# Kernel optimization log

Hardware: AMD Instinct MI355X
Metric: run time of the kernel (lower is better)

## Reference

```python
import jax, jax.numpy as jnp
import numpy as np

B, S, BERT_H = 8, 512, 432
NL, HD = 12, 64
H = NL * HD  # 768
NEG = -1e12

def _lin(k, i, o):
    return jax.random.normal(k, (i, o), jnp.float32) * 0.02

def setup_inputs():
    key = jax.random.key(0)
    ks = jax.random.split(key, 12)
    return {
        "bert_hidden": jax.random.normal(ks[0], (B, S, BERT_H), jnp.float32),
        "attention_mask": jnp.ones((B, S), jnp.float32),
        "dense_w": _lin(ks[1], BERT_H, H), "dense_b": jnp.zeros((H,)),
        "sat_qw": _lin(ks[2], H, H), "sat_qb": jnp.zeros((H,)),
        "sat_kw": _lin(ks[3], H, H), "sat_kb": jnp.zeros((H,)),
        "sat_vw": _lin(ks[4], H, H), "sat_vb": jnp.zeros((H,)),
        "sat_ow": _lin(ks[5], H, H), "sat_ob": jnp.zeros((H,)),
        "rel_qw": _lin(ks[6], H, H), "rel_qb": jnp.zeros((H,)),
        "rel_kw": _lin(ks[7], H, H), "rel_kb": jnp.zeros((H,)),
        "rel_vw": _lin(ks[8], H, H), "rel_vb": jnp.zeros((H,)),
        "rel_ow": _lin(ks[9], H, H), "rel_ob": jnp.zeros((H,)),
        "lns_w": jnp.ones((H,)), "lns_b": jnp.zeros((H,)),
        "lnr_w": jnp.ones((H,)), "lnr_b": jnp.zeros((H,)),
        "head_w": _lin(ks[10], H, 2 * HD), "head_b": jnp.zeros((2 * HD,)),
        "tail_w": _lin(ks[11], 2 * HD, 2 * NL), "tail_b": jnp.zeros((2 * NL,)),
    }

def _layernorm(x, w, b, eps=1e-12):
    u = x.mean(-1, keepdims=True)
    s = ((x - u) ** 2).mean(-1, keepdims=True)
    return w * (x - u) / jnp.sqrt(s + eps) + b

def _mha(q_in, k_in, v_in, wq, bq, wk, bk, wv, bv, wo, bo):
    # q_in: [N, Lq, H]; k_in/v_in: [N, Lk, H]; dropout is identity (eval)
    N, Lq, _ = q_in.shape
    Lk = k_in.shape[1]
    qh = (q_in @ wq + bq).reshape(N, Lq, NL, HD)
    kh = (k_in @ wk + bk).reshape(N, Lk, NL, HD)
    vh = (v_in @ wv + bv).reshape(N, Lk, NL, HD)
    scores = jnp.einsum('nqhd,nkhd->nhqk', qh, kh) / np.float32(np.sqrt(HD))
    probs = jax.nn.softmax(scores, axis=-1)
    ctx = jnp.einsum('nhqk,nkhd->nqhd', probs, vh).reshape(N, Lq, NL * HD)
    return ctx @ wo + bo + q_in

def _shift_back(x):
    # faithful torch cycle_shift(forward=False): circular roll left by 1
    return jnp.roll(x, -1, axis=1)

def _shift_fwd(x):
    # faithful to the torch sequential in-place loop in cycle_shift(forward=True):
    # out[0] = x[-1]; out[1:] = x[0] (each copy reads the already-overwritten slot)
    b, s, h = x.shape
    return jnp.concatenate([x[:, -1:, :], jnp.broadcast_to(x[:, :1, :], (b, s - 1, h))], axis=1)

def reference(bert_hidden, attention_mask, dense_w, dense_b,
              sat_qw, sat_qb, sat_kw, sat_kb, sat_vw, sat_vb, sat_ow, sat_ob,
              rel_qw, rel_qb, rel_kw, rel_kb, rel_vw, rel_vb, rel_ow, rel_ob,
              lns_w, lns_b, lnr_w, lnr_b, head_w, head_b, tail_w, tail_b):
    hidden0 = bert_hidden @ dense_w + dense_b  # [B,S,H]
    cs = hidden0
    center = cs.mean(axis=1)  # [B,H], avg_pool2d over seq dim
    for _ in range(2):
        before = _shift_back(cs)
        after = _shift_fwd(cs)
        center_exp = jnp.broadcast_to(center[:, None, :], cs.shape)
        concats = jnp.stack([before, cs, after, hidden0, center_exp], axis=2)  # [B,S,5,H]
        concats = concats.reshape(B * S, 5, H)
        q = cs.reshape(B * S, 1, H)
        sat = _mha(q, concats, concats, sat_qw, sat_qb, sat_kw, sat_kb, sat_vw, sat_vb, sat_ow, sat_ob)
        cs = _layernorm(jax.nn.relu(sat), lns_w, lns_b).reshape(B, S, H)
        cc = jnp.concatenate([center[:, None, :], cs], axis=1)  # [B,S+1,H]
        rel = _mha(center[:, None, :], cc, cc, rel_qw, rel_qb, rel_kw, rel_kb, rel_vw, rel_vb, rel_ow, rel_ob)
        center = _layernorm(jax.nn.relu(rel), lnr_w, lnr_b)[:, 0, :]
    outputs = cs @ head_w + head_b  # [B,S,2*HD]
    qw, kw = outputs[..., ::2], outputs[..., 1::2]  # [B,S,HD]
    pos = jnp.arange(S, dtype=jnp.float32)
    inv = jnp.power(10000.0, -2.0 * jnp.arange(HD // 2, dtype=jnp.float32) / HD)
    ang = pos[:, None] * inv[None, :]  # [S,HD//2]
    pe = jnp.stack([jnp.sin(ang), jnp.cos(ang)], axis=-1).reshape(S, HD)
    cos_pos = jnp.repeat(pe[:, 1::2], 2, axis=-1)  # [S,HD]
    sin_pos = jnp.repeat(pe[:, ::2], 2, axis=-1)
    def rot(x):
        x2 = jnp.stack([-x[..., 1::2], x[..., ::2]], axis=-1).reshape(x.shape)
        return x * cos_pos + x2 * sin_pos
    qw, kw = rot(qw), rot(kw)
    logits = jnp.einsum('bmd,bnd->bmn', qw, kw) / np.float32(np.sqrt(HD))  # [B,S,S]
    bias = jnp.einsum('bnh->bhn', outputs @ tail_w + tail_b) / 2.0  # [B,2*NL,S]
    logits = logits[:, None, :, :] + bias[:, ::2, None, :] + bias[:, 1::2, :, None]  # [B,NL,S,S]
    m1 = attention_mask[:, None, :, None]
    logits = logits * m1 + NEG * (1.0 - m1)
    m2 = attention_mask[:, None, None, :]
    logits = logits * m2 + NEG * (1.0 - m2)
    tril = jnp.tril(jnp.ones((S, S), logits.dtype), k=-1)
    return logits - tril * 1e12
```

## Files before the change

### kernel.cpp

```cpp
#include <hip/hip_runtime.h>
#include <cstdint>
#include <cstddef>

#define HH 768
#define SS 512
#define NBATCH 8
#define NLH 12
#define HDIM 64
#define BSROWS 4096
static constexpr float NEGV = -1000000000000.0f;

typedef unsigned short ushort_t;
typedef __attribute__((ext_vector_type(4))) float fx4;
typedef __attribute__((ext_vector_type(8))) short sx8;

__device__ __forceinline__ ushort_t f2bf(float f) {
  uint32_t u = __float_as_uint(f);
  uint32_t r = (u + 0x7FFFu + ((u >> 16) & 1u)) >> 16;
  return (ushort_t)r;
}
__device__ __forceinline__ float bf2f(ushort_t h) {
  return __uint_as_float(((uint32_t)h) << 16);
}
__device__ __forceinline__ float2 ldbf2(const ushort_t* p) {
  uint32_t u = *(const uint32_t*)p;
  return make_float2(__uint_as_float(u << 16), __uint_as_float(u & 0xffff0000u));
}

__device__ __forceinline__ void async_copy16(void* lds, const void* g) {
  __builtin_amdgcn_global_load_lds(
      (const __attribute__((address_space(1))) void*)g,
      (__attribute__((address_space(3))) void*)lds, 16, 0, 0);
}

__global__ __launch_bounds__(256) void gemm_bf16(
    const ushort_t* __restrict__ A, int lda,
    const ushort_t* __restrict__ B, int ldb,
    const float* __restrict__ bias,
    const ushort_t* __restrict__ resb,
    ushort_t* __restrict__ Cb, int ldo,
    ushort_t* __restrict__ Cb2, int ldo2, int nsplit, int K, int nx,
    float* __restrict__ colmean)
{
  __shared__ ushort_t As[128 * 64];
  __shared__ ushort_t Bs[128 * 64];
  const int tid = threadIdx.x;
  const int nwg = gridDim.x;
  const int q = nwg >> 3;
  const int xcd = blockIdx.x & 7, sidx = blockIdx.x >> 3;
  const int swz = xcd * q + sidx;
  const int bm = (swz / nx) * 128;
  const int bn = (swz % nx) * 128;
  const int l = tid & 63;
  const int w = tid >> 6;
  const int wr = w >> 1, wc = w & 1;
  const int r8 = tid >> 3;
  const int sl = tid & 7;

  fx4 acc[4][4];
#pragma unroll
  for (int m = 0; m < 4; ++m)
#pragma unroll
    for (int n = 0; n < 4; ++n) acc[m][n] = (fx4)0.f;

  for (int k0 = 0; k0 < K; k0 += 64) {
#pragma unroll
    for (int i = 0; i < 4; ++i) {
      int row = i * 32 + r8;
      int srcs = sl ^ (row & 7);
      async_copy16((char*)As + i * 4096 + tid * 16,
                   A + (size_t)(bm + row) * lda + k0 + srcs * 8);
    }
#pragma unroll
    for (int i = 0; i < 4; ++i) {
      int row = i * 32 + r8;
      int srcs = sl ^ (row & 7);
      async_copy16((char*)Bs + i * 4096 + tid * 16,
                   B + (size_t)(bn + row) * ldb + k0 + srcs * 8);
    }
    __syncthreads();
#pragma unroll
    for (int kk = 0; kk < 2; ++kk) {
      sx8 av[4], bv[4];
      const int so = (l >> 4) + kk * 4;
#pragma unroll
      for (int m = 0; m < 4; ++m) {
        int r = wr * 64 + m * 16 + (l & 15);
        av[m] = *(const sx8*)((const char*)As + r * 128 + ((so ^ (r & 7)) * 16));
      }
#pragma unroll
      for (int n = 0; n < 4; ++n) {
        int r = wc * 64 + n * 16 + (l & 15);
        bv[n] = *(const sx8*)((const char*)Bs + r * 128 + ((so ^ (r & 7)) * 16));
      }
#pragma unroll
      for (int m = 0; m < 4; ++m)
#pragma unroll
        for (int n = 0; n < 4; ++n)
          acc[m][n] = __builtin_amdgcn_mfma_f32_16x16x32_bf16(av[m], bv[n], acc[m][n], 0, 0, 0);
    }
    __syncthreads();
  }

  const bool second = (bn >= nsplit);
  ushort_t* dst = second ? Cb2 : Cb;
  const int ld = second ? ldo2 : ldo;
  const int csub = second ? nsplit : 0;
  const int cr0 = bm + wr * 64 + (l >> 4) * 4;
  const int cc0 = bn + wc * 64 + (l & 15);
#pragma unroll
  for (int m = 0; m < 4; ++m) {
#pragma unroll
    for (int n = 0; n < 4; ++n) {
      int col = cc0 + n * 16;
      float bcol = bias[col];
#pragma unroll
      for (int j = 0; j < 4; ++j) {
        int row = cr0 + m * 16 + j;
        size_t off = (size_t)row * ld + (col - csub);
        float v = acc[m][n][j] + bcol;
        if (resb) v += bf2f(resb[off]);
        dst[off] = f2bf(v);
      }
    }
  }

  if (colmean) {
    float* scr = (float*)As;
    const int cid = wr * 4 + (l >> 4);
#pragma unroll
    for (int n = 0; n < 4; ++n) {
      int colL = wc * 64 + n * 16 + (l & 15);
      float t = 16.0f * bias[bn + colL];
#pragma unroll
      for (int m = 0; m < 4; ++m)
#pragma unroll
        for (int j = 0; j < 4; ++j) t += acc[m][n][j];
      scr[cid * 128 + colL] = t;
    }
    __syncthreads();
    if (tid < 128) {
      float scol = 0.f;
#pragma unroll
      for (int c = 0; c < 8; ++c) scol += scr[c * 128 + tid];
      atomicAdd(&colmean[(bm >> 9) * HH + bn + tid], scol * (1.0f / 512.0f));
    }
  }
}

__global__ __launch_bounds__(256) void head_fused(
    const ushort_t* __restrict__ A,
    const ushort_t* __restrict__ B,
    const float* __restrict__ head_b,
    const float* __restrict__ tail_w,
    const float* __restrict__ tail_b,
    float* __restrict__ qw, float* __restrict__ kw,
    float* __restrict__ bias2)
{
  __shared__ ushort_t As[128 * 64];
  __shared__ ushort_t Bs[128 * 64];
  __shared__ float tile[128][130];
  __shared__ float invt[32];
  const int tid = threadIdx.x;
  const int bm = blockIdx.x * 128;
  const int l = tid & 63;
  const int w = tid >> 6;
  const int wr = w >> 1, wc = w & 1;
  const int r8 = tid >> 3;
  const int sl = tid & 7;

  if (tid < 32) invt[tid] = powf(10000.0f, -(float)tid / 32.0f);

  fx4 acc[4][4];
#pragma unroll
  for (int m = 0; m < 4; ++m)
#pragma unroll
    for (int n = 0; n < 4; ++n) acc[m][n] = (fx4)0.f;

  for (int k0 = 0; k0 < HH; k0 += 64) {
#pragma unroll
    for (int i = 0; i < 4; ++i) {
      int row = i * 32 + r8;
      int srcs = sl ^ (row & 7);
      async_copy16((char*)As + i * 4096 + tid * 16,
                   A + (size_t)(bm + row) * HH + k0 + srcs * 8);
    }
#pragma unroll
    for (int i = 0; i < 4; ++i) {
      int row = i * 32 + r8;
      int srcs = sl ^ (row & 7);
      async_copy16((char*)Bs + i * 4096 + tid * 16,
                   B + (size_t)row * HH + k0 + srcs * 8);
    }
    __syncthreads();
#pragma unroll
    for (int kk = 0; kk < 2; ++kk) {
      sx8 av[4], bv[4];
      const int so = (l >> 4) + kk * 4;
#pragma unroll
      for (int m = 0; m < 4; ++m) {
        int r = wr * 64 + m * 16 + (l & 15);
        av[m] = *(const sx8*)((const char*)As + r * 128 + ((so ^ (r & 7)) * 16));
      }
#pragma unroll
      for (int n = 0; n < 4; ++n) {
        int r = wc * 64 + n * 16 + (l & 15);
        bv[n] = *(const sx8*)((const char*)Bs + r * 128 + ((so ^ (r & 7)) * 16));
      }
#pragma unroll
      for (int m = 0; m < 4; ++m)
#pragma unroll
        for (int n = 0; n < 4; ++n)
          acc[m][n] = __builtin_amdgcn_mfma_f32_16x16x32_bf16(av[m], bv[n], acc[m][n], 0, 0, 0);
    }
    __syncthreads();
  }

  const int cr0 = wr * 64 + (l >> 4) * 4;
  const int cc0 = wc * 64 + (l & 15);
#pragma unroll
  for (int m = 0; m < 4; ++m)
#pragma unroll
    for (int n = 0; n < 4; ++n) {
      int col = cc0 + n * 16;
      float bcol = head_b[col];
#pragma unroll
      for (int j = 0; j < 4; ++j)
        tile[cr0 + m * 16 + j][col] = acc[m][n][j] + bcol;
    }
  __syncthreads();

  for (int t = tid; t < 128 * 32; t += 256) {
    int r = t >> 5, i = t & 31;
    int s = (bm + r) & 511;
    float ang = (float)s * invt[i];
    float sn = sinf(ang), cn = cosf(ang);
    float q0 = tile[r][4 * i + 0], k0 = tile[r][4 * i + 1];
    float q1 = tile[r][4 * i + 2], k1 = tile[r][4 * i + 3];
    float* qp = qw + (size_t)(bm + r) * 64 + i * 2;
    float* kp = kw + (size_t)(bm + r) * 64 + i * 2;
    qp[0] = q0 * cn - q1 * sn; qp[1] = q1 * cn + q0 * sn;
    kp[0] = k0 * cn - k1 * sn; kp[1] = k1 * cn + k0 * sn;
  }
  for (int t = tid; t < 128 * 24; t += 256) {
    int r = t / 24, c = t % 24;
    float acc2 = tail_b[c];
#pragma unroll 16
    for (int k = 0; k < 128; ++k) acc2 = fmaf(tile[r][k], tail_w[k * 24 + c], acc2);
    bias2[(size_t)(bm + r) * 24 + c] = acc2 * 0.5f;
  }
}

struct TJob { const float* src; ushort_t* dst; int K, N, Kpad, rowOff; };
struct PrepArgs {
  TJob j[8];
  const float* bert; ushort_t* bert_bf;
  const float* rkb; const float* rvb; const float* sqb; const float* skb; const float* svb;
  float* b_merged;
  float* center;
};
__global__ __launch_bounds__(256) void prep_all(PrepArgs pa)
{
  if (blockIdx.z < 8) {
    TJob jb = pa.j[blockIdx.z];
    int k0 = blockIdx.x * 32, n0 = blockIdx.y * 32;
    if (k0 >= jb.Kpad || n0 >= jb.N) return;
    __shared__ float t[32][33];
    int tx = threadIdx.x & 31, ty = threadIdx.x >> 5;
#pragma unroll
    for (int i = 0; i < 4; ++i) {
      int k = k0 + ty + i * 8;
      float v = 0.f;
      if (k < jb.K && n0 + tx < jb.N) v = jb.src[(size_t)k * jb.N + n0 + tx];
      t[ty + i * 8][tx] = v;
    }
    __syncthreads();
#pragma unroll
    for (int i = 0; i < 4; ++i) {
      int n = n0 + ty + i * 8;
      int k = k0 + tx;
      if (n < jb.N && k < jb.Kpad)
        jb.dst[(size_t)(jb.rowOff + n) * jb.Kpad + k] = f2bf(t[tx][ty + i * 8]);
    }
  } else {
    const int NB = BSROWS * 448;
    const int total = NB + 3840 + NBATCH * HH;
    int start = (blockIdx.y * 24 + blockIdx.x) * 256 + threadIdx.x;
    for (int i = start; i < total; i += 24 * 24 * 256) {
      if (i < NB) {
        int r = i / 448, c = i % 448;
        pa.bert_bf[i] = (c < 432) ? f2bf(pa.bert[(size_t)r * 432 + c]) : (ushort_t)0;
      } else if (i < NB + 3840) {
        int c = i - NB;
        float v;
        if (c < 768) v = pa.rkb[c];
        else if (c < 1536) v = pa.rvb[c - 768];
        else if (c < 2304) v = pa.sqb[c - 1536];
        else if (c < 3072) v = pa.skb[c - 2304];
        else v = pa.svb[c - 3072];
        pa.b_merged[c] = v;
      } else {
        pa.center[i - NB - 3840] = 0.f;
      }
    }
  }
}

struct SmallJob { const float* W; const float* bias; const float* res; float* C; };
struct SmallJobs { SmallJob j[5]; };
__global__ __launch_bounds__(256) void gemm_skinny(
    const float* __restrict__ A, SmallJobs jobs)
{
  __shared__ float As[8 * HH];
  __shared__ float part[8 * 8 * 32];
  const int tid = threadIdx.x;
  const SmallJob job = jobs.j[blockIdx.y];
#pragma unroll
  for (int i = 0; i < 6; ++i) {
    int idx = tid * 4 + i * 1024;
    *(float4*)&As[idx] = *(const float4*)(A + idx);
  }
  __syncthreads();
  const int c = tid & 31;
  const int col = (blockIdx.x << 5) + c;
  const int ks = tid >> 5;
  const float* Wp = job.W + (size_t)(ks * 96) * HH + col;
  float acc[8] = {};
#pragma unroll 8
  for (int k = 0; k < 96; ++k) {
    float wv = Wp[(size_t)k * HH];
    const float* ap = &As[ks * 96 + k];
#pragma unroll
    for (int m = 0; m < 8; ++m)
      acc[m] = fmaf(ap[m * HH], wv, acc[m]);
  }
#pragma unroll
  for (int m = 0; m < 8; ++m)
    part[ks * 256 + m * 32 + c] = acc[m];
  __syncthreads();
  const int m = tid >> 5;
  const int c2 = tid & 31;
  float s = 0.f;
#pragma unroll
  for (int k = 0; k < 8; ++k) s += part[k * 256 + m * 32 + c2];
  const int outcol = (blockIdx.x << 5) + c2;
  float v = s + job.bias[outcol];
  if (job.res) v += job.res[(size_t)m * HH + outcol];
  job.C[(size_t)m * HH + outcol] = v;
}

struct SmallJobs2 { SmallJob j[2]; };
__global__ __launch_bounds__(256) void skinny_ln(
    const float* __restrict__ relo, const float* __restrict__ lw, const float* __restrict__ lb,
    SmallJobs2 jobs)
{
  __shared__ float As[8 * HH];
  __shared__ float part[8 * 8 * 32];
  const int tid = threadIdx.x;
  const SmallJob job = jobs.j[blockIdx.y];
#pragma unroll
  for (int i = 0; i < 6; ++i) {
    int idx = tid * 4 + i * 1024;
    *(float4*)&As[idx] = *(const float4*)(relo + idx);
  }
  __syncthreads();
  {
    const int row = tid >> 5, lc = tid & 31;
    float s = 0.f, sq = 0.f;
#pragma unroll
    for (int e = 0; e < 24; ++e) {
      float x = fmaxf(As[row * HH + lc * 24 + e], 0.f);
      s += x; sq += x * x;
    }
#pragma unroll
    for (int d = 1; d < 32; d <<= 1) { s += __shfl_xor(s, d); sq += __shfl_xor(sq, d); }
    float mean = s * (1.0f / HH);
    float var = sq * (1.0f / HH) - mean * mean;
    float rstd = rsqrtf(var + 1e-12f);
#pragma unroll
    for (int e = 0; e < 24; ++e) {
      int cc = lc * 24 + e;
      float x = fmaxf(As[row * HH + cc], 0.f);
      As[row * HH + cc] = lw[cc] * (x - mean) * rstd + lb[cc];
    }
  }
  __syncthreads();
  const int c = tid & 31;
  const int col = (blockIdx.x << 5) + c;
  const int ks = tid >> 5;
  const float* Wp = job.W + (size_t)(ks * 96) * HH + col;
  float acc[8] = {};
#pragma unroll 8
  for (int k = 0; k < 96; ++k) {
    float wv = Wp[(size_t)k * HH];
    const float* ap = &As[ks * 96 + k];
#pragma unroll
    for (int m = 0; m < 8; ++m)
      acc[m] = fmaf(ap[m * HH], wv, acc[m]);
  }
#pragma unroll
  for (int m = 0; m < 8; ++m)
    part[ks * 256 + m * 32 + c] = acc[m];
  __syncthreads();
  const int m = tid >> 5;
  const int c2 = tid & 31;
  float s2 = 0.f;
#pragma unroll
  for (int k = 0; k < 8; ++k) s2 += part[k * 256 + m * 32 + c2];
  const int outcol = (blockIdx.x << 5) + c2;
  job.C[(size_t)m * HH + outcol] = s2 + job.bias[outcol];
}

__global__ __launch_bounds__(256) void sat_attn(
    const ushort_t* __restrict__ Qc, const ushort_t* __restrict__ Kc,
    const ushort_t* __restrict__ Vc, int ldq,
    const ushort_t* __restrict__ Kh0, const ushort_t* __restrict__ Vh0, int ldh,
    const float* __restrict__ Kcen, const float* __restrict__ Vcen,
    ushort_t* __restrict__ ctxb)
{
  int i = blockIdx.x;
  int b = i >> 9, s = i & 511;
  int lane = threadIdx.x & 63;
  int wave = threadIdx.x >> 6;
  size_t rb = (size_t)(b * SS + ((s + 1) & 511));
  size_t rs = (size_t)i;
  size_t ra = (size_t)(b * SS + (s == 0 ? (SS - 1) : 0));
  size_t rc = (size_t)b * HH;
  const int half = lane >> 5;
  const int d0 = (lane & 31) * 2;
#pragma unroll
  for (int it = 0; it < 2; ++it) {
    int p = wave + 4 * it;
    if (p >= 6) break;
    int off = (2 * p + half) * HDIM + d0;
    float2 q  = ldbf2(Qc + rs * ldq + off);
    float2 kb = ldbf2(Kc + rb * ldq + off);
    float2 ks = ldbf2(Kc + rs * ldq + off);
    float2 ka = ldbf2(Kc + ra * ldq + off);
    float2 kh = ldbf2(Kh0 + rs * ldh + off);
    float2 kc = *(const float2*)(Kcen + rc + off);
    float s0 = q.x * kb.x + q.y * kb.y;
    float s1 = q.x * ks.x + q.y * ks.y;
    float s2 = q.x * ka.x + q.y * ka.y;
    float s3 = q.x * kh.x + q.y * kh.y;
    float s4 = q.x * kc.x + q.y * kc.y;
#pragma unroll
    for (int d = 1; d < 32; d <<= 1) {
      s0 += __shfl_xor(s0, d); s1 += __shfl_xor(s1, d); s2 += __shfl_xor(s2, d);
      s3 += __shfl_xor(s3, d); s4 += __shfl_xor(s4, d);
    }
    const float sc = 0.125f;
    s0 *= sc; s1 *= sc; s2 *= sc; s3 *= sc; s4 *= sc;
    float mx = fmaxf(fmaxf(fmaxf(s0, s1), fmaxf(s2, s3)), s4);
    float e0 = __expf(s0 - mx), e1 = __expf(s1 - mx), e2 = __expf(s2 - mx);
    float e3 = __expf(s3 - mx), e4 = __expf(s4 - mx);
    float inv = 1.f / (e0 + e1 + e2 + e3 + e4);
    float2 vb = ldbf2(Vc + rb * ldq + off);
    float2 vs = ldbf2(Vc + rs * ldq + off);
    float2 va = ldbf2(Vc + ra * ldq + off);
    float2 vh = ldbf2(Vh0 + rs * ldh + off);
    float2 vc = *(const float2*)(Vcen + rc + off);
    float vx = e0 * vb.x + e1 * vs.x + e2 * va.x + e3 * vh.x + e4 * vc.x;
    float vy = e0 * vb.y + e1 * vs.y + e2 * va.y + e3 * vh.y + e4 * vc.y;
    uint32_t o = (uint32_t)f2bf(vx * inv) | ((uint32_t)f2bf(vy * inv) << 16);
    *(uint32_t*)(ctxb + rs * HH + off) = o;
  }
}

__global__ __launch_bounds__(256) void relu_ln_bf(
    const ushort_t* __restrict__ x, const float* __restrict__ w, const float* __restrict__ b,
    ushort_t* __restrict__ ybf)
{
  int row = blockIdx.x;
  const ushort_t* xr = x + (size_t)row * HH;
  float v[3];
  float sum = 0.f, sumsq = 0.f;
#pragma unroll
  for (int j = 0; j < 3; ++j) {
    float t = bf2f(xr[threadIdx.x + j * 256]);
    t = fmaxf(t, 0.f);
    v[j] = t;
    sum += t; sumsq += t * t;
  }
#pragma unroll
  for (int d = 1; d < 64; d <<= 1) { sum += __shfl_xor(sum, d); sumsq += __shfl_xor(sumsq, d); }
  __shared__ float ws_[4], wsq_[4];
  int wave = threadIdx.x >> 6, lane = threadIdx.x & 63;
  if (lane == 0) { ws_[wave] = sum; wsq_[wave] = sumsq; }
  __syncthreads();
  sum = ws_[0] + ws_[1] + ws_[2] + ws_[3];
  sumsq = wsq_[0] + wsq_[1] + wsq_[2] + wsq_[3];
  float mean = sum * (1.0f / HH);
  float var = sumsq * (1.0f / HH) - mean * mean;
  float rstd = rsqrtf(var + 1e-12f);
#pragma unroll
  for (int j = 0; j < 3; ++j) {
    int cidx = threadIdx.x + j * 256;
    float o = w[cidx] * (v[j] - mean) * rstd + b[cidx];
    ybf[(size_t)row * HH + cidx] = f2bf(o);
  }
}

__global__ __launch_bounds__(256) void rel_attn(
    const float* __restrict__ Qr, const float* __restrict__ Krc, const ushort_t* __restrict__ Kr,
    const float* __restrict__ Vrc, const ushort_t* __restrict__ Vr, int ldkv,
    float* __restrict__ ctx)
{
  int b = blockIdx.x, h = blockIdx.y;
  __shared__ float qs[64];
  __shared__ float sc[513];
  __shared__ float part[4][64];
  __shared__ float redm[4], redsum[4];
  int t = threadIdx.x, lane = t & 63, wave = t >> 6;
  if (t < 64) qs[t] = Qr[b * HH + h * HDIM + t];
  __syncthreads();
  for (int j = t; j < 513; j += 256) {
    float acc = 0.f;
    if (j == 0) {
      const float* kp = Krc + b * HH + h * HDIM;
#pragma unroll
      for (int d = 0; d < HDIM; ++d) acc = fmaf(qs[d], kp[d], acc);
    } else {
      const sx8* kv = (const sx8*)(Kr + (size_t)(b * SS + j - 1) * ldkv + h * HDIM);
#pragma unroll
      for (int dq = 0; dq < 8; ++dq) {
        sx8 v = kv[dq];
#pragma unroll
        for (int e = 0; e < 8; ++e)
          acc = fmaf(qs[dq * 8 + e], bf2f((ushort_t)v[e]), acc);
      }
    }
    sc[j] = acc * 0.125f;
  }
  __syncthreads();
  float m = -1e30f;
  for (int j = t; j < 513; j += 256) m = fmaxf(m, sc[j]);
#pragma unroll
  for (int d = 1; d < 64; d <<= 1) m = fmaxf(m, __shfl_xor(m, d));
  if (lane == 0) redm[wave] = m;
  __syncthreads();
  m = fmaxf(fmaxf(redm[0], redm[1]), fmaxf(redm[2], redm[3]));
  float lsum = 0.f;
  for (int j = t; j < 513; j += 256) { float e = __expf(sc[j] - m); sc[j] = e; lsum += e; }
#pragma unroll
  for (int d = 1; d < 64; d <<= 1) lsum += __shfl_xor(lsum, d);
  if (lane == 0) redsum[wave] = lsum;
  __syncthreads();
  float total = redsum[0] + redsum[1] + redsum[2] + redsum[3];
  float accv = 0.f;
#pragma unroll 8
  for (int j = wave; j < 513; j += 4) {
    float vv = (j == 0) ? Vrc[b * HH + h * HDIM + lane]
                        : bf2f(Vr[(size_t)(b * SS + j - 1) * ldkv + h * HDIM + lane]);
    accv = fmaf(sc[j], vv, accv);
  }
  part[wave][lane] = accv;
  __syncthreads();
  if (wave == 0) {
    float r = (part[0][lane] + part[1][lane] + part[2][lane] + part[3][lane]) / total;
    ctx[b * HH + h * HDIM + lane] = r;
  }
}

__global__ __launch_bounds__(256) void final_kernel(
    const float* __restrict__ qw, const float* __restrict__ kw,
    const float* __restrict__ bias2, const float* __restrict__ mask,
    float* __restrict__ out)
{
  int b = blockIdx.z;
  int mt = blockIdx.y * 32;
  int nt = blockIdx.x * 32;
  __shared__ float qs[32][68];
  __shared__ float ks[32][68];
  int t = threadIdx.x;
  {
    int idx = t * 8;
    int r = idx >> 6, c = idx & 63;
    const float* sq = qw + (size_t)(b * SS + mt + r) * 64 + c;
    const float* sk = kw + (size_t)(b * SS + nt + r) * 64 + c;
    *(float4*)&qs[r][c]     = *(const float4*)(sq);
    *(float4*)&qs[r][c + 4] = *(const float4*)(sq + 4);
    *(float4*)&ks[r][c]     = *(const float4*)(sk);
    *(float4*)&ks[r][c + 4] = *(const float4*)(sk + 4);
  }
  __syncthreads();
  int m = t >> 3;
  int n0 = (t & 7) * 4;
  float d0 = 0.f, d1 = 0.f, d2 = 0.f, d3 = 0.f;
#pragma unroll
  for (int d = 0; d < 64; d += 4) {
    float4 qv = *(const float4*)&qs[m][d];
    float4 k0 = *(const float4*)&ks[n0 + 0][d];
    float4 k1 = *(const float4*)&ks[n0 + 1][d];
    float4 k2 = *(const float4*)&ks[n0 + 2][d];
    float4 k3 = *(const float4*)&ks[n0 + 3][d];
    d0 += qv.x * k0.x + qv.y * k0.y + qv.z * k0.z + qv.w * k0.w;
    d1 += qv.x * k1.x + qv.y * k1.y + qv.z * k1.z + qv.w * k1.w;
    d2 += qv.x * k2.x + qv.y * k2.y + qv.z * k2.z + qv.w * k2.w;
    d3 += qv.x * k3.x + qv.y * k3.y + qv.z * k3.z + qv.w * k3.w;
  }
  int gm = mt + m;
  int gn = nt + n0;
  d0 *= 0.125f; d1 *= 0.125f; d2 *= 0.125f; d3 *= 0.125f;
  float mm = mask[b * SS + gm];
  float mn0 = mask[b * SS + gn + 0];
  float mn1 = mask[b * SS + gn + 1];
  float mn2 = mask[b * SS + gn + 2];
  float mn3 = mask[b * SS + gn + 3];
  const float* bmp  = bias2 + (size_t)(b * SS + gm) * 24;
  const float* bnp0 = bias2 + (size_t)(b * SS + gn + 0) * 24;
  const float* bnp1 = bias2 + (size_t)(b * SS + gn + 1) * 24;
  const float* bnp2 = bias2 + (size_t)(b * SS + gn + 2) * 24;
  const float* bnp3 = bias2 + (size_t)(b * SS + gn + 3) * 24;
// ... 54 lines not shown
  char*  ws  = (char*)d_ws;

  size_t off = 0;
  auto alloc = [&](size_t bytes) { char* p = ws + off; off += (bytes + 255) & ~(size_t)255; return p; };
  ushort_t* bert_bf   = (ushort_t*)alloc((size_t)BSROWS * 448 * 2);
  ushort_t* Wt_dense  = (ushort_t*)alloc((size_t)768 * 448 * 2);
  ushort_t* Wt_big    = (ushort_t*)alloc((size_t)3840 * 768 * 2);
  ushort_t* Wt_satow  = (ushort_t*)alloc((size_t)768 * 768 * 2);
  ushort_t* Wt_head   = (ushort_t*)alloc((size_t)128 * 768 * 2);
  ushort_t* hidden0_bf= (ushort_t*)alloc((size_t)BSROWS * HH * 2);
  ushort_t* ctx_bf    = (ushort_t*)alloc((size_t)BSROWS * HH * 2);
  ushort_t* csA_bf    = (ushort_t*)alloc((size_t)BSROWS * HH * 2);
  float* b_merged = (float*)alloc(3840 * 4);
  float* center   = (float*)alloc(6144 * 4);
  float* Kcen     = (float*)alloc(6144 * 4);
  float* Vcen     = (float*)alloc(6144 * 4);
  float* Qr       = (float*)alloc(6144 * 4);
  float* Krc      = (float*)alloc(6144 * 4);
  float* Vrc      = (float*)alloc(6144 * 4);
  float* ctxr     = (float*)alloc(6144 * 4);
  float* relo     = (float*)alloc(6144 * 4);
  float* bias2    = (float*)alloc((size_t)BSROWS * 24 * 4);
  float* qwbuf    = (float*)alloc((size_t)BSROWS * 64 * 4);
  float* kwbuf    = (float*)alloc((size_t)BSROWS * 64 * 4);

  ushort_t* QKV1_bf = (ushort_t*)out;
  ushort_t* tmp1_bf = QKV1_bf + (size_t)BSROWS * 2304;
  ushort_t* KrVr_bf = tmp1_bf + (size_t)BSROWS * 768;
  ushort_t* QKV2_bf = KrVr_bf + (size_t)BSROWS * 1536;
  ushort_t* tmp2_bf = tmp1_bf;

  dim3 blk(256);

  {
    PrepArgs pa;
    pa.j[0] = { dense_w, Wt_dense, 432, 768, 448, 0 };
    pa.j[1] = { rel_kw,  Wt_big,   768, 768, 768, 0 };
    pa.j[2] = { rel_vw,  Wt_big,   768, 768, 768, 768 };
    pa.j[3] = { sat_qw,  Wt_big,   768, 768, 768, 1536 };
    pa.j[4] = { sat_kw,  Wt_big,   768, 768, 768, 2304 };
    pa.j[5] = { sat_vw,  Wt_big,   768, 768, 768, 3072 };
    pa.j[6] = { sat_ow,  Wt_satow, 768, 768, 768, 0 };
    pa.j[7] = { head_w,  Wt_head,  768, 128, 768, 0 };
    pa.bert = bert; pa.bert_bf = bert_bf;
    pa.rkb = rel_kb; pa.rvb = rel_vb; pa.sqb = sat_qb; pa.skb = sat_kb; pa.svb = sat_vb;
    pa.b_merged = b_merged; pa.center = center;
    prep_all<<<dim3(24, 24, 9), blk, 0, stream>>>(pa);
  }

  gemm_bf16<<<dim3(192), blk, 0, stream>>>(bert_bf, 448, Wt_dense, 448, dense_b,
                                           nullptr, hidden0_bf, HH,
                                           nullptr, 0, 1 << 30, 448, 6, center);

  gemm_bf16<<<dim3(576), blk, 0, stream>>>(hidden0_bf, HH, Wt_big + (size_t)1536 * 768, HH,
                                           b_merged + 1536, nullptr, QKV1_bf, 2304,
                                           nullptr, 0, 1 << 30, HH, 18, nullptr);
  {
    SmallJobs jobs;
    jobs.j[0] = { sat_kw, sat_kb, nullptr, Kcen };
    jobs.j[1] = { sat_vw, sat_vb, nullptr, Vcen };
    jobs.j[2] = { rel_qw, rel_qb, nullptr, Qr };
    jobs.j[3] = { rel_kw, rel_kb, nullptr, Krc };
    jobs.j[4] = { rel_vw, rel_vb, nullptr, Vrc };
    gemm_skinny<<<dim3(24, 5), blk, 0, stream>>>(center, jobs);
  }
  sat_attn<<<BSROWS, 256, 0, stream>>>(QKV1_bf, QKV1_bf + 768, QKV1_bf + 1536, 2304,
                                       QKV1_bf + 768, QKV1_bf + 1536, 2304,
                                       Kcen, Vcen, ctx_bf);
  gemm_bf16<<<dim3(192), blk, 0, stream>>>(ctx_bf, HH, Wt_satow, HH, sat_ob,
                                           hidden0_bf, tmp1_bf, HH,
                                           nullptr, 0, 1 << 30, HH, 6, nullptr);
  relu_ln_bf<<<BSROWS, 256, 0, stream>>>(tmp1_bf, lns_w, lns_b, csA_bf);

  gemm_bf16<<<dim3(960), blk, 0, stream>>>(csA_bf, HH, Wt_big, HH, b_merged,
                                           nullptr, KrVr_bf, 1536,
                                           QKV2_bf, 2304, 1536, HH, 30, nullptr);
  rel_attn<<<dim3(8, 12), 256, 0, stream>>>(Qr, Krc, KrVr_bf, Vrc, KrVr_bf + 768, 1536, ctxr);
  {
    SmallJobs jobs;
    jobs.j[0] = { rel_ow, rel_ob, center, relo };
    gemm_skinny<<<dim3(24, 1), blk, 0, stream>>>(ctxr, jobs);
  }
  {
    SmallJobs2 jobs;
    jobs.j[0] = { sat_kw, sat_kb, nullptr, Kcen };
    jobs.j[1] = { sat_vw, sat_vb, nullptr, Vcen };
    skinny_ln<<<dim3(24, 2), blk, 0, stream>>>(relo, lnr_w, lnr_b, jobs);
  }
  sat_attn<<<BSROWS, 256, 0, stream>>>(QKV2_bf, QKV2_bf + 768, QKV2_bf + 1536, 2304,
                                       QKV1_bf + 768, QKV1_bf + 1536, 2304,
                                       Kcen, Vcen, ctx_bf);
  gemm_bf16<<<dim3(192), blk, 0, stream>>>(ctx_bf, HH, Wt_satow, HH, sat_ob,
                                           csA_bf, tmp2_bf, HH,
                                           nullptr, 0, 1 << 30, HH, 6, nullptr);
  relu_ln_bf<<<BSROWS, 256, 0, stream>>>(tmp2_bf, lns_w, lns_b, csA_bf);

  head_fused<<<32, blk, 0, stream>>>(csA_bf, Wt_head, head_b, tail_w, tail_b,
                                     qwbuf, kwbuf, bias2);
  final_kernel<<<dim3(16, 16, 8), 256, 0, stream>>>(qwbuf, kwbuf, bias2, amask, out);
}
```

Measured before the change: 311.8 us.

## Merge QKV GEMM with skinny center GEMMs and fuse final ReLU-LayerNorm into head GEMM

The large QKV GEMM and the five skinny center-row GEMMs now run in one launch. Their shared bodies are factored into device functions, and the block index decides which path a block takes. The last relu_ln_bf launch is removed: head_fused computes per-row mean and rstd from the raw residual sum itself and normalizes its A tile while loading it into LDS. This saves two kernel launches and one full-activation round trip. In exchange, the A operand in head_fused uses synchronous loads plus ALU work instead of async LDS copies, and the merged kernel shares one LDS arena between two differently shaped paths.

```diff
diff --git a/kernel.cpp b/kernel.cpp
--- a/kernel.cpp
+++ b/kernel.cpp
@@ -31,6 +31,166 @@
   __builtin_amdgcn_global_load_lds(
       (const __attribute__((address_space(1))) void*)g,
       (__attribute__((address_space(3))) void*)lds, 16, 0, 0);
+}
+
+__device__ __forceinline__ void gemm_core(
+    char* arena, int bid, int nwg, int nx,
+    const ushort_t* __restrict__ A, int lda,
+    const ushort_t* __restrict__ B, int ldb,
+    const float* __restrict__ bias,
+    const ushort_t* __restrict__ resb,
+    ushort_t* __restrict__ Cb, int ldo,
+    ushort_t* __restrict__ Cb2, int ldo2, int nsplit, int K,
+    float* __restrict__ colmean)
+{
+  ushort_t* As = (ushort_t*)arena;
+  ushort_t* Bs = (ushort_t*)(arena + 16384);
+  const int tid = threadIdx.x;
+  const int q = nwg >> 3;
+  const int xcd = bid & 7, sidx = bid >> 3;
+  const int swz = xcd * q + sidx;
+  const int bm = (swz / nx) * 128;
+  const int bn = (swz % nx) * 128;
+  const int l = tid & 63;
+  const int w = tid >> 6;
+  const int wr = w >> 1, wc = w & 1;
+  const int r8 = tid >> 3;
+  const int sl = tid & 7;
+
+  fx4 acc[4][4];
+#pragma unroll
+  for (int m = 0; m < 4; ++m)
+#pragma unroll
+    for (int n = 0; n < 4; ++n) acc[m][n] = (fx4)0.f;
+
+  for (int k0 = 0; k0 < K; k0 += 64) {
+#pragma unroll
+    for (int i = 0; i < 4; ++i) {
+      int row = i * 32 + r8;
+      int srcs = sl ^ (row & 7);
+      async_copy16((char*)As + i * 4096 + tid * 16,
+                   A + (size_t)(bm + row) * lda + k0 + srcs * 8);
+    }
+#pragma unroll
+    for (int i = 0; i < 4; ++i) {
+      int row = i * 32 + r8;
+      int srcs = sl ^ (row & 7);
+      async_copy16((char*)Bs + i * 4096 + tid * 16,
+                   B + (size_t)(bn + row) * ldb + k0 + srcs * 8);
+    }
+    __syncthreads();
+#pragma unroll
+    for (int kk = 0; kk < 2; ++kk) {
+      sx8 av[4], bv[4];
+      const int so = (l >> 4) + kk * 4;
+#pragma unroll
+      for (int m = 0; m < 4; ++m) {
+        int r = wr * 64 + m * 16 + (l & 15);
+        av[m] = *(const sx8*)((const char*)As + r * 128 + ((so ^ (r & 7)) * 16));
+      }
+#pragma unroll
+      for (int n = 0; n < 4; ++n) {
+        int r = wc * 64 + n * 16 + (l & 15);
+        bv[n] = *(const sx8*)((const char*)Bs + r * 128 + ((so ^ (r & 7)) * 16));
+      }
+#pragma unroll
+      for (int m = 0; m < 4; ++m)
+#pragma unroll
+        for (int n = 0; n < 4; ++n)
+          acc[m][n] = __builtin_amdgcn_mfma_f32_16x16x32_bf16(av[m], bv[n], acc[m][n], 0, 0, 0);
+    }
+    __syncthreads();
+  }
+
+  const bool second = (bn >= nsplit);
+  ushort_t* dst = second ? Cb2 : Cb;
+  const int ld = second ? ldo2 : ldo;
+  const int csub = second ? nsplit : 0;
+  const int cr0 = bm + wr * 64 + (l >> 4) * 4;
+  const int cc0 = bn + wc * 64 + (l & 15);
+#pragma unroll
+  for (int m = 0; m < 4; ++m) {
+#pragma unroll
+    for (int n = 0; n < 4; ++n) {
+      int col = cc0 + n * 16;
+      float bcol = bias[col];
+#pragma unroll
+      for (int j = 0; j < 4; ++j) {
+        int row = cr0 + m * 16 + j;
+        size_t off = (size_t)row * ld + (col - csub);
+        float v = acc[m][n][j] + bcol;
+        if (resb) v += bf2f(resb[off]);
+        dst[off] = f2bf(v);
+      }
+    }
+  }
+
+  if (colmean) {
+    float* scr = (float*)arena;
+    const int cid = wr * 4 + (l >> 4);
+#pragma unroll
+    for (int n = 0; n < 4; ++n) {
+      int colL = wc * 64 + n * 16 + (l & 15);
+      float t = 16.0f * bias[bn + colL];
+#pragma unroll
+      for (int m = 0; m < 4; ++m)
+#pragma unroll
+        for (int j = 0; j < 4; ++j) t += acc[m][n][j];
+      scr[cid * 128 + colL] = t;
+    }
+    __syncthreads();
+    if (tid < 128) {
+      float scol = 0.f;
+#pragma unroll
+      for (int c = 0; c < 8; ++c) scol += scr[c * 128 + tid];
+      atomicAdd(&colmean[(bm >> 9) * HH + bn + tid], scol * (1.0f / 512.0f));
+    }
+  }
+}
+
+struct SmallJob { const float* W; const float* bias; const float* res; float* C; };
+struct SmallJobs { SmallJob j[5]; };
+
+__device__ __forceinline__ void skinny_core(
+    char* arena, int colblk,
+    const float* __restrict__ A, const float* __restrict__ W,
+    const float* __restrict__ bias, const float* __restrict__ res, float* __restrict__ C)
+{
+  float* As = (float*)arena;
+  float* part = (float*)(arena + 24576);
+  const int tid = threadIdx.x;
+#pragma unroll
+  for (int i = 0; i < 6; ++i) {
+    int idx = tid * 4 + i * 1024;
+    *(float4*)&As[idx] = *(const float4*)(A + idx);
+  }
+  __syncthreads();
+  const int c = tid & 31;
+  const int col = (colblk << 5) + c;
+  const int ks = tid >> 5;
+  const float* Wp = W + (size_t)(ks * 96) * HH + col;
+  float acc[8] = {};
+#pragma unroll 8
+  for (int k = 0; k < 96; ++k) {
+    float wv = Wp[(size_t)k * HH];
+    const float* ap = &As[ks * 96 + k];
+#pragma unroll
+    for (int m = 0; m < 8; ++m)
+      acc[m] = fmaf(ap[m * HH], wv, acc[m]);
+  }
+#pragma unroll
+  for (int m = 0; m < 8; ++m)
+    part[ks * 256 + m * 32 + c] = acc[m];
+  __syncthreads();
+  const int m = tid >> 5;
+  const int c2 = tid & 31;
+  float s = 0.f;
+#pragma unroll
+  for (int k = 0; k < 8; ++k) s += part[k * 256 + m * 32 + c2];
+  const int outcol = (colblk << 5) + c2;
+  float v = s + bias[outcol];
+  if (res) v += res[(size_t)m * HH + outcol];
+  C[(size_t)m * HH + outcol] = v;
 }
 
 __global__ __launch_bounds__(256) void gemm_bf16(
@@ -42,114 +202,161 @@
     ushort_t* __restrict__ Cb2, int ldo2, int nsplit, int K, int nx,
     float* __restrict__ colmean)
 {
-  __shared__ ushort_t As[128 * 64];
-  __shared__ ushort_t Bs[128 * 64];
+  __shared__ char arena[32768];
+  gemm_core(arena, blockIdx.x, gridDim.x, nx, A, lda, B, ldb, bias, resb,
+            Cb, ldo, Cb2, ldo2, nsplit, K, colmean);
+}
+
+__global__ __launch_bounds__(256) void qkv_center(
+    const ushort_t* __restrict__ A, const ushort_t* __restrict__ B,
+    const float* __restrict__ bias, ushort_t* __restrict__ Cb,
+    SmallJobs jobs, const float* __restrict__ center)
+{
+  __shared__ char arena[32768];
+  if (blockIdx.x < 576) {
+    gemm_core(arena, blockIdx.x, 576, 18, A, HH, B, HH, bias, nullptr,
+              Cb, 2304, nullptr, 0, 1 << 30, HH, nullptr);
+  } else {
+    int vb = blockIdx.x - 576;
+    SmallJob jb = jobs.j[vb / 24];
+    skinny_core(arena, vb % 24, center, jb.W, jb.bias, jb.res, jb.C);
+  }
+}
+
+__global__ __launch_bounds__(256) void gemm_skinny(
+    const float* __restrict__ A, SmallJobs jobs)
+{
+  __shared__ char arena[32768];
+  SmallJob jb = jobs.j[blockIdx.y];
+  skinny_core(arena, blockIdx.x, A, jb.W, jb.bias, jb.res, jb.C);
+}
+
+struct SmallJobs2 { SmallJob j[2]; };
+__global__ __launch_bounds__(256) void skinny_ln(
+    const float* __restrict__ relo, const float* __restrict__ lw, const float* __restrict__ lb,
+    SmallJobs2 jobs)
+{
+  __shared__ float As[8 * HH];
+  __shared__ float part[8 * 8 * 32];
   const int tid = threadIdx.x;
-  const int nwg = gridDim.x;
-  const int q = nwg >> 3;
-  const int xcd = blockIdx.x & 7, sidx = blockIdx.x >> 3;
-  const int swz = xcd * q + sidx;
-  const int bm = (swz / nx) * 128;
-  const int bn = (swz % nx) * 128;
-  const int l = tid & 63;
-  const int w = tid >> 6;
-  const int wr = w >> 1, wc = w & 1;
-  const int r8 = tid >> 3;
-  const int sl = tid & 7;
-
-  fx4 acc[4][4];
-#pragma unroll
-  for (int m = 0; m < 4; ++m)
-#pragma unroll
-    for (int n = 0; n < 4; ++n) acc[m][n] = (fx4)0.f;
-
-  for (int k0 = 0; k0 < K; k0 += 64) {
-#pragma unroll
-    for (int i = 0; i < 4; ++i) {
-      int row = i * 32 + r8;
-      int srcs = sl ^ (row & 7);
-      async_copy16((char*)As + i * 4096 + tid * 16,
-                   A + (size_t)(bm + row) * lda + k0 + srcs * 8);
-    }
-#pragma unroll
-    for (int i = 0; i < 4; ++i) {
-      int row = i * 32 + r8;
-      int srcs = sl ^ (row & 7);
-      async_copy16((char*)Bs + i * 4096 + tid * 16,
-                   B + (size_t)(bn + row) * ldb + k0 + srcs * 8);
-    }
-    __syncthreads();
-#pragma unroll
-    for (int kk = 0; kk < 2; ++kk) {
-      sx8 av[4], bv[4];
-      const int so = (l >> 4) + kk * 4;
-#pragma unroll
-      for (int m = 0; m < 4; ++m) {
-        int r = wr * 64 + m * 16 + (l & 15);
-        av[m] = *(const sx8*)((const char*)As + r * 128 + ((so ^ (r & 7)) * 16));
+  const SmallJob job = jobs.j[blockIdx.y];
+#pragma unroll
+  for (int i = 0; i < 6; ++i) {
+    int idx = tid * 4 + i * 1024;
+    *(float4*)&As[idx] = *(const float4*)(relo + idx);
+  }
+  __syncthreads();
+  {
+    const int row = tid >> 5, lc = tid & 31;
+    float s = 0.f, sq = 0.f;
+#pragma unroll
+    for (int e = 0; e < 24; ++e) {
+      float x = fmaxf(As[row * HH + lc * 24 + e], 0.f);
+      s += x; sq += x * x;
+    }
+#pragma unroll
+    for (int d = 1; d < 32; d <<= 1) { s += __shfl_xor(s, d); sq += __shfl_xor(sq, d); }
+    float mean = s * (1.0f / HH);
+    float var = sq * (1.0f / HH) - mean * mean;
+    float rstd = rsqrtf(var + 1e-12f);
+#pragma unroll
+    for (int e = 0; e < 24; ++e) {
+      int cc = lc * 24 + e;
+      float x = fmaxf(As[row * HH + cc], 0.f);
+      As[row * HH + cc] = lw[cc] * (x - mean) * rstd + lb[cc];
+    }
+  }
+  __syncthreads();
+  const int c = tid & 31;
+  const int col = (blockIdx.x << 5) + c;
+  const int ks = tid >> 5;
+  const float* Wp = job.W + (size_t)(ks * 96) * HH + col;
+  float acc[8] = {};
+#pragma unroll 8
+  for (int k = 0; k < 96; ++k) {
+    float wv = Wp[(size_t)k * HH];
+    const float* ap = &As[ks * 96 + k];
+#pragma unroll
+    for (int m = 0; m < 8; ++m)
+      acc[m] = fmaf(ap[m * HH], wv, acc[m]);
+  }
+#pragma unroll
+  for (int m = 0; m < 8; ++m)
+    part[ks * 256 + m * 32 + c] = acc[m];
+  __syncthreads();
+  const int m = tid >> 5;
+  const int c2 = tid & 31;
+  float s2 = 0.f;
+#pragma unroll
+  for (int k = 0; k < 8; ++k) s2 += part[k * 256 + m * 32 + c2];
+  const int outcol = (blockIdx.x << 5) + c2;
+  job.C[(size_t)m * HH + outcol] = s2 + job.bias[outcol];
+}
+
+__global__ __launch_bounds__(256) void rel_attn(
+    const float* __restrict__ Qr, const float* __restrict__ Krc, const ushort_t* __restrict__ Kr,
+    const float* __restrict__ Vrc, const ushort_t* __restrict__ Vr, int ldkv,
+    float* __restrict__ ctx)
+{
+  int b = blockIdx.x, h = blockIdx.y;
+  __shared__ float qs[64];
+  __shared__ float sc[513];
+  __shared__ float part[4][64];
+  __shared__ float redm[4], redsum[4];
+  int t = threadIdx.x, lane = t & 63, wave = t >> 6;
+  if (t < 64) qs[t] = Qr[b * HH + h * HDIM + t];
+  __syncthreads();
+  for (int j = t; j < 513; j += 256) {
+    float acc = 0.f;
+    if (j == 0) {
+      const float* kp = Krc + b * HH + h * HDIM;
+#pragma unroll
+      for (int d = 0; d < HDIM; ++d) acc = fmaf(qs[d], kp[d], acc);
+    } else {
+      const sx8* kv = (const sx8*)(Kr + (size_t)(b * SS + j - 1) * ldkv + h * HDIM);
+#pragma unroll
+      for (int dq = 0; dq < 8; ++dq) {
+        sx8 v = kv[dq];
+#pragma unroll
+        for (int e = 0; e < 8; ++e)
+          acc = fmaf(qs[dq * 8 + e], bf2f((ushort_t)v[e]), acc);
       }
-#pragma unroll
-      for (int n = 0; n < 4; ++n) {
-        int r = wc * 64 + n * 16 + (l & 15);
-        bv[n] = *(const sx8*)((const char*)Bs + r * 128 + ((so ^ (r & 7)) * 16));
-      }
-#pragma unroll
-      for (int m = 0; m < 4; ++m)
-#pragma unroll
-        for (int n = 0; n < 4; ++n)
-          acc[m][n] = __builtin_amdgcn_mfma_f32_16x16x32_bf16(av[m], bv[n], acc[m][n], 0, 0, 0);
-    }
-    __syncthreads();
-  }
-
-  const bool second = (bn >= nsplit);
-  ushort_t* dst = second ? Cb2 : Cb;
-  const int ld = second ? ldo2 : ldo;
-  const int csub = second ? nsplit : 0;
-  const int cr0 = bm + wr * 64 + (l >> 4) * 4;
-  const int cc0 = bn + wc * 64 + (l & 15);
-#pragma unroll
-  for (int m = 0; m < 4; ++m) {
-#pragma unroll
-    for (int n = 0; n < 4; ++n) {
-      int col = cc0 + n * 16;
-      float bcol = bias[col];
-#pragma unroll
-      for (int j = 0; j < 4; ++j) {
-        int row = cr0 + m * 16 + j;
-        size_t off = (size_t)row * ld + (col - csub);
-        float v = acc[m][n][j] + bcol;
-        if (resb) v += bf2f(resb[off]);
-        dst[off] = f2bf(v);
-      }
-    }
-  }
-
-  if (colmean) {
-    float* scr = (float*)As;
-    const int cid = wr * 4 + (l >> 4);
-#pragma unroll
-    for (int n = 0; n < 4; ++n) {
-      int colL = wc * 64 + n * 16 + (l & 15);
-      float t = 16.0f * bias[bn + colL];
-#pragma unroll
-      for (int m = 0; m < 4; ++m)
-#pragma unroll
-        for (int j = 0; j < 4; ++j) t += acc[m][n][j];
-      scr[cid * 128 + colL] = t;
-    }
-    __syncthreads();
-    if (tid < 128) {
-      float scol = 0.f;
-#pragma unroll
-      for (int c = 0; c < 8; ++c) scol += scr[c * 128 + tid];
-      atomicAdd(&colmean[(bm >> 9) * HH + bn + tid], scol * (1.0f / 512.0f));
-    }
+    }
+    sc[j] = acc * 0.125f;
+  }
+  __syncthreads();
+  float m = -1e30f;
+  for (int j = t; j < 513; j += 256) m = fmaxf(m, sc[j]);
+#pragma unroll
+  for (int d = 1; d < 64; d <<= 1) m = fmaxf(m, __shfl_xor(m, d));
+  if (lane == 0) redm[wave] = m;
+  __syncthreads();
+  m = fmaxf(fmaxf(redm[0], redm[1]), fmaxf(redm[2], redm[3]));
+  float lsum = 0.f;
+  for (int j = t; j < 513; j += 256) { float e = __expf(sc[j] - m); sc[j] = e; lsum += e; }
+#pragma unroll
+  for (int d = 1; d < 64; d <<= 1) lsum += __shfl_xor(lsum, d);
+  if (lane == 0) redsum[wave] = lsum;
+  __syncthreads();
+  float total = redsum[0] + redsum[1] + redsum[2] + redsum[3];
+  float accv = 0.f;
+#pragma unroll 8
+  for (int j = wave; j < 513; j += 4) {
+    float vv = (j == 0) ? Vrc[b * HH + h * HDIM + lane]
+                        : bf2f(Vr[(size_t)(b * SS + j - 1) * ldkv + h * HDIM + lane]);
+    accv = fmaf(sc[j], vv, accv);
+  }
+  part[wave][lane] = accv;
+  __syncthreads();
+  if (wave == 0) {
+    float r = (part[0][lane] + part[1][lane] + part[2][lane] + part[3][lane]) / total;
+    ctx[b * HH + h * HDIM + lane] = r;
   }
 }
 
 __global__ __launch_bounds__(256) void head_fused(
-    const ushort_t* __restrict__ A,
+    const ushort_t* __restrict__ Araw,
+    const float* __restrict__ lnw, const float* __restrict__ lnb,
     const ushort_t* __restrict__ B,
     const float* __restrict__ head_b,
     const float* __restrict__ tail_w,
@@ -161,6 +368,7 @@
   __shared__ ushort_t Bs[128 * 64];
   __shared__ float tile[128][130];
   __shared__ float invt[32];
+  __shared__ float2 rst[128];
   const int tid = threadIdx.x;
   const int bm = blockIdx.x * 128;
   const int l = tid & 63;
@@ -171,6 +379,28 @@
 
   if (tid < 32) invt[tid] = powf(10000.0f, -(float)tid / 32.0f);
 
+  {
+    int row = tid >> 1, half = tid & 1;
+    const ushort_t* rp = Araw + (size_t)(bm + row) * HH + half * 384;
+    float s = 0.f, sq = 0.f;
+#pragma unroll 8
+    for (int c = 0; c < 48; ++c) {
+      sx8 v = *(const sx8*)(rp + c * 8);
+#pragma unroll
+      for (int e = 0; e < 8; ++e) {
+        float x = fmaxf(bf2f((ushort_t)v[e]), 0.f);
+        s += x; sq += x * x;
+      }
+    }
+    s += __shfl_xor(s, 1); sq += __shfl_xor(sq, 1);
+    if (half == 0) {
+      float mean = s * (1.0f / HH);
+      float var = sq * (1.0f / HH) - mean * mean;
+      rst[row] = make_float2(mean, rsqrtf(var + 1e-12f));
+    }
+  }
+  __syncthreads();
+
   fx4 acc[4][4];
 #pragma unroll
   for (int m = 0; m < 4; ++m)
@@ -178,13 +408,6 @@
     for (int n = 0; n < 4; ++n) acc[m][n] = (fx4)0.f;
 
   for (int k0 = 0; k0 < HH; k0 += 64) {
-#pragma unroll
-    for (int i = 0; i < 4; ++i) {
-      int row = i * 32 + r8;
-      int srcs = sl ^ (row & 7);
-      async_copy16((char*)As + i * 4096 + tid * 16,
-                   A + (size_t)(bm + row) * HH + k0 + srcs * 8);
-    }
 #pragma unroll
     for (int i = 0; i < 4; ++i) {
       int row = i * 32 + r8;
@@ -192,10 +415,31 @@
       async_copy16((char*)Bs + i * 4096 + tid * 16,
                    B + (size_t)row * HH + k0 + srcs * 8);
     }
+#pragma unroll
+    for (int i = 0; i < 4; ++i) {
+      int row = i * 32 + r8;
+      int slot = sl ^ (row & 7);
+      int gk = k0 + slot * 8;
+      sx8 v = *(const sx8*)(Araw + (size_t)(bm + row) * HH + gk);
+      float4 w0 = *(const float4*)(lnw + gk);
+      float4 w1 = *(const float4*)(lnw + gk + 4);
+      float4 b0 = *(const float4*)(lnb + gk);
+      float4 b1 = *(const float4*)(lnb + gk + 4);
+      float wv[8] = {w0.x, w0.y, w0.z, w0.w, w1.x, w1.y, w1.z, w1.w};
+      float bv[8] = {b0.x, b0.y, b0.z, b0.w, b1.x, b1.y, b1.z, b1.w};
+      float2 mr = rst[row];
+      sx8 ov;
+#pragma unroll
+      for (int e = 0; e < 8; ++e) {
+        float x = fmaxf(bf2f((ushort_t)v[e]), 0.f);
+        ov[e] = (short)f2bf(fmaf((x - mr.x) * mr.y, wv[e], bv[e]));
+      }
+      *(sx8*)((char*)As + i * 4096 + tid * 16) = ov;
+    }
     __syncthreads();
 #pragma unroll
     for (int kk = 0; kk < 2; ++kk) {
-      sx8 av[4], bv[4];
+      sx8 av[4], bvv[4];
       const int so = (l >> 4) + kk * 4;
 #pragma unroll
       for (int m = 0; m < 4; ++m) {
@@ -205,13 +449,13 @@
 #pragma unroll
       for (int n = 0; n < 4; ++n) {
         int r = wc * 64 + n * 16 + (l & 15);
-        bv[n] = *(const sx8*)((const char*)Bs + r * 128 + ((so ^ (r & 7)) * 16));
+        bvv[n] = *(const sx8*)((const char*)Bs + r * 128 + ((so ^ (r & 7)) * 16));
       }
 #pragma unroll
       for (int m = 0; m < 4; ++m)
 #pragma unroll
         for (int n = 0; n < 4; ++n)
-          acc[m][n] = __builtin_amdgcn_mfma_f32_16x16x32_bf16(av[m], bv[n], acc[m][n], 0, 0, 0);
+          acc[m][n] = __builtin_amdgcn_mfma_f32_16x16x32_bf16(av[m], bvv[n], acc[m][n], 0, 0, 0);
     }
     __syncthreads();
   }
@@ -306,111 +550,6 @@
   }
 }
 
-struct SmallJob { const float* W; const float* bias; const float* res; float* C; };
-struct SmallJobs { SmallJob j[5]; };
-__global__ __launch_bounds__(256) void gemm_skinny(
-    const float* __restrict__ A, SmallJobs jobs)
-{
-  __shared__ float As[8 * HH];
-  __shared__ float part[8 * 8 * 32];
-  const int tid = threadIdx.x;
-  const SmallJob job = jobs.j[blockIdx.y];
-#pragma unroll
-  for (int i = 0; i < 6; ++i) {
-    int idx = tid * 4 + i * 1024;
-    *(float4*)&As[idx] = *(const float4*)(A + idx);
-  }
-  __syncthreads();
-  const int c = tid & 31;
-  const int col = (blockIdx.x << 5) + c;
-  const int ks = tid >> 5;
-  const float* Wp = job.W + (size_t)(ks * 96) * HH + col;
-  float acc[8] = {};
-#pragma unroll 8
-  for (int k = 0; k < 96; ++k) {
-    float wv = Wp[(size_t)k * HH];
-    const float* ap = &As[ks * 96 + k];
-#pragma unroll
-    for (int m = 0; m < 8; ++m)
-      acc[m] = fmaf(ap[m * HH], wv, acc[m]);
-  }
-#pragma unroll
-  for (int m = 0; m < 8; ++m)
-    part[ks * 256 + m * 32 + c] = acc[m];
-  __syncthreads();
-  const int m = tid >> 5;
-  const int c2 = tid & 31;
-  float s = 0.f;
-#pragma unroll
-  for (int k = 0; k < 8; ++k) s += part[k * 256 + m * 32 + c2];
-  const int outcol = (blockIdx.x << 5) + c2;
-  float v = s + job.bias[outcol];
-  if (job.res) v += job.res[(size_t)m * HH + outcol];
-  job.C[(size_t)m * HH + outcol] = v;
-}
-
-struct SmallJobs2 { SmallJob j[2]; };
-__global__ __launch_bounds__(256) void skinny_ln(
-    const float* __restrict__ relo, const float* __restrict__ lw, const float* __restrict__ lb,
-    SmallJobs2 jobs)
-{
-  __shared__ float As[8 * HH];
-  __shared__ float part[8 * 8 * 32];
-  const int tid = threadIdx.x;
-  const SmallJob job = jobs.j[blockIdx.y];
-#pragma unroll
-  for (int i = 0; i < 6; ++i) {
-    int idx = tid * 4 + i * 1024;
-    *(float4*)&As[idx] = *(const float4*)(relo + idx);
-  }
-  __syncthreads();
-  {
-    const int row = tid >> 5, lc = tid & 31;
-    float s = 0.f, sq = 0.f;
-#pragma unroll
-    for (int e = 0; e < 24; ++e) {
-      float x = fmaxf(As[row * HH + lc * 24 + e], 0.f);
-      s += x; sq += x * x;
-    }
-#pragma unroll
-    for (int d = 1; d < 32; d <<= 1) { s += __shfl_xor(s, d); sq += __shfl_xor(sq, d); }
-    float mean = s * (1.0f / HH);
-    float var = sq * (1.0f / HH) - mean * mean;
-    float rstd = rsqrtf(var + 1e-12f);
-#pragma unroll
-    for (int e = 0; e < 24; ++e) {
-      int cc = lc * 24 + e;
-      float x = fmaxf(As[row * HH + cc], 0.f);
-      As[row * HH + cc] = lw[cc] * (x - mean) * rstd + lb[cc];
-    }
-  }
-  __syncthreads();
-  const int c = tid & 31;
-  const int col = (blockIdx.x << 5) + c;
-  const int ks = tid >> 5;
-  const float* Wp = job.W + (size_t)(ks * 96) * HH + col;
-  float acc[8] = {};
-#pragma unroll 8
-  for (int k = 0; k < 96; ++k) {
-    float wv = Wp[(size_t)k * HH];
-    const float* ap = &As[ks * 96 + k];
-#pragma unroll
-    for (int m = 0; m < 8; ++m)
-      acc[m] = fmaf(ap[m * HH], wv, acc[m]);
-  }
-#pragma unroll
-  for (int m = 0; m < 8; ++m)
-    part[ks * 256 + m * 32 + c] = acc[m];
-  __syncthreads();
-  const int m = tid >> 5;
-  const int c2 = tid & 31;
-  float s2 = 0.f;
-#pragma unroll
-  for (int k = 0; k < 8; ++k) s2 += part[k * 256 + m * 32 + c2];
-  const int outcol = (blockIdx.x << 5) + c2;
-  job.C[(size_t)m * HH + outcol] = s2 + job.bias[outcol];
-}
-
 __global__ __launch_bounds__(256) void sat_attn(
     const ushort_t* __restrict__ Qc, const ushort_t* __restrict__ Kc,
     const ushort_t* __restrict__ Vc, int ldq,
@@ -498,67 +637,6 @@
     int cidx = threadIdx.x + j * 256;
     float o = w[cidx] * (v[j] - mean) * rstd + b[cidx];
     ybf[(size_t)row * HH + cidx] = f2bf(o);
-  }
-}
-
-__global__ __launch_bounds__(256) void rel_attn(
-    const float* __restrict__ Qr, const float* __restrict__ Krc, const ushort_t* __restrict__ Kr,
-    const float* __restrict__ Vrc, const ushort_t* __restrict__ Vr, int ldkv,
-    float* __restrict__ ctx)
-{
-  int b = blockIdx.x, h = blockIdx.y;
-  __shared__ float qs[64];
-  __shared__ float sc[513];
-  __shared__ float part[4][64];
-  __shared__ float redm[4], redsum[4];
-  int t = threadIdx.x, lane = t & 63, wave = t >> 6;
-  if (t < 64) qs[t] = Qr[b * HH + h * HDIM + t];
-  __syncthreads();
-  for (int j = t; j < 513; j += 256) {
-    float acc = 0.f;
-    if (j == 0) {
-      const float* kp = Krc + b * HH + h * HDIM;
-#pragma unroll
-      for (int d = 0; d < HDIM; ++d) acc = fmaf(qs[d], kp[d], acc);
-    } else {
-      const sx8* kv = (const sx8*)(Kr + (size_t)(b * SS + j - 1) * ldkv + h * HDIM);
-#pragma unroll
-      for (int dq = 0; dq < 8; ++dq) {
-        sx8 v = kv[dq];
-#pragma unroll
-        for (int e = 0; e < 8; ++e)
-          acc = fmaf(qs[dq * 8 + e], bf2f((ushort_t)v[e]), acc);
-      }
-    }
-    sc[j] = acc * 0.125f;
-  }
-  __syncthreads();
-  float m = -1e30f;
-  for (int j = t; j < 513; j += 256) m = fmaxf(m, sc[j]);
-#pragma unroll
-  for (int d = 1; d < 64; d <<= 1) m = fmaxf(m, __shfl_xor(m, d));
-  if (lane == 0) redm[wave] = m;
-  __syncthreads();
-  m = fmaxf(fmaxf(redm[0], redm[1]), fmaxf(redm[2], redm[3]));
-  float lsum = 0.f;
-  for (int j = t; j < 513; j += 256) { float e = __expf(sc[j] - m); sc[j] = e; lsum += e; }
-#pragma unroll
-  for (int d = 1; d < 64; d <<= 1) lsum += __shfl_xor(lsum, d);
-  if (lane == 0) redsum[wave] = lsum;
-  __syncthreads();
-  float total = redsum[0] + redsum[1] + redsum[2] + redsum[3];
-  float accv = 0.f;
-#pragma unroll 8
-  for (int j = wave; j < 513; j += 4) {
-    float vv = (j == 0) ? Vrc[b * HH + h * HDIM + lane]
-                        : bf2f(Vr[(size_t)(b * SS + j - 1) * ldkv + h * HDIM + lane]);
-    accv = fmaf(sc[j], vv, accv);
-  }
-  part[wave][lane] = accv;
-  __syncthreads();
-  if (wave == 0) {
-    float r = (part[0][lane] + part[1][lane] + part[2][lane] + part[3][lane]) / total;
-    ctx[b * HH + h * HDIM + lane] = r;
   }
 }
 
@@ -719,9 +797,6 @@
                                            nullptr, hidden0_bf, HH,
                                            nullptr, 0, 1 << 30, 448, 6, center);
 
-  gemm_bf16<<<dim3(576), blk, 0, stream>>>(hidden0_bf, HH, Wt_big + (size_t)1536 * 768, HH,
-                                           b_merged + 1536, nullptr, QKV1_bf, 2304,
-                                           nullptr, 0, 1 << 30, HH, 18, nullptr);
   {
     SmallJobs jobs;
     jobs.j[0] = { sat_kw, sat_kb, nullptr, Kcen };
@@ -729,7 +804,8 @@
     jobs.j[2] = { rel_qw, rel_qb, nullptr, Qr };
     jobs.j[3] = { rel_kw, rel_kb, nullptr, Krc };
     jobs.j[4] = { rel_vw, rel_vb, nullptr, Vrc };
-    gemm_skinny<<<dim3(24, 5), blk, 0, stream>>>(center, jobs);
+    qkv_center<<<dim3(696), blk, 0, stream>>>(hidden0_bf, Wt_big + (size_t)1536 * 768,
+                                              b_merged + 1536, QKV1_bf, jobs, center);
   }
   sat_attn<<<BSROWS, 256, 0, stream>>>(QKV1_bf, QKV1_bf + 768, QKV1_bf + 1536, 2304,
                                        QKV1_bf + 768, QKV1_bf + 1536, 2304,
@@ -760,9 +836,7 @@
   gemm_bf16<<<dim3(192), blk, 0, stream>>>(ctx_bf, HH, Wt_satow, HH, sat_ob,
                                            csA_bf, tmp2_bf, HH,
                                            nullptr, 0, 1 << 30, HH, 6, nullptr);
-  relu_ln_bf<<<BSROWS, 256, 0, stream>>>(tmp2_bf, lns_w, lns_b, csA_bf);
-
-  head_fused<<<32, blk, 0, stream>>>(csA_bf, Wt_head, head_b, tail_w, tail_b,
-                                     qwbuf, kwbuf, bias2);
+  head_fused<<<32, blk, 0, stream>>>(tmp2_bf, lns_w, lns_b, Wt_head, head_b,
+                                     tail_w, tail_b, qwbuf, kwbuf, bias2);
   final_kernel<<<dim3(16, 16, 8), 256, 0, stream>>>(qwbuf, kwbuf, bias2, amask, out);
 }
```

After: 306.7 us. Within noise of the previous version (-1.6%).
